# Kernel tuning notes

Measured on AMD Instinct MI355X. Metric: run time of the kernel, lower is better.

Reference implementation:

```python
import jax, jax.numpy as jnp
import numpy as np

NEG_SLOPE = 0.2


def gat_conv(x, edge_index, W, a_src, a_dst, b, heads, ch, concat):
    # PyG GATConv (eval mode, add_self_loops=True).
    # x: [N, Fin]; W: [Fin, heads*ch]; a_src/a_dst: [heads, ch]; b: [heads*ch] or [ch]
    N = x.shape[0]
    loop = jnp.arange(N, dtype=edge_index.dtype)
    src = jnp.concatenate([edge_index[0], loop])
    dst = jnp.concatenate([edge_index[1], loop])
    h = (x @ W).reshape(N, heads, ch)                     # [N,H,C]
    s_src = jnp.sum(h * a_src, axis=-1)                   # [N,H]
    s_dst = jnp.sum(h * a_dst, axis=-1)                   # [N,H]
    e = jax.nn.leaky_relu(s_src[src] + s_dst[dst], NEG_SLOPE)  # [E,H]
    # numerically stable softmax over incoming edges of each dst node
    emax = jax.lax.stop_gradient(jax.ops.segment_max(e, dst, num_segments=N))
    ex = jnp.exp(e - emax[dst])
    denom = jax.ops.segment_sum(ex, dst, num_segments=N) + 1e-16
    alpha = ex / denom[dst]                                # [E,H]
    out = jax.ops.segment_sum(alpha[:, :, None] * h[src], dst, num_segments=N)  # [N,H,C]
    out = out.reshape(N, heads * ch) if concat else out.mean(axis=1)
    return out + b


def setup_inputs() -> dict:
    key = jax.random.key(0)
    N, E, Fin, H, C = 50000, 800000, 64, 8, 16
    D1 = H * C            # 128
    D2 = 3 * D1           # 384
    ks = jax.random.split(key, 40)
    d = {}
    d["X"] = jax.random.normal(ks[0], (N, Fin), dtype=jnp.float32)
    d["A1"] = jax.random.randint(ks[1], (2, E), 0, N, dtype=jnp.int32)
    d["A2"] = jax.random.randint(ks[2], (2, E), 0, N, dtype=jnp.int32)
    d["A3"] = jax.random.randint(ks[3], (2, E), 0, N, dtype=jnp.int32)
    d["edge_feature"] = jax.random.normal(ks[4], (E, 2), dtype=jnp.float32)
    i = 5
    for branch in (1, 2, 3):
        d[f"W{branch}1"] = jax.random.normal(ks[i], (Fin, D1), dtype=jnp.float32) * 0.1; i += 1
        d[f"a_src{branch}1"] = jax.random.normal(ks[i], (H, C), dtype=jnp.float32) * 0.1; i += 1
        d[f"a_dst{branch}1"] = jax.random.normal(ks[i], (H, C), dtype=jnp.float32) * 0.1; i += 1
        d[f"b{branch}1"] = jnp.zeros((D1,), dtype=jnp.float32)
        d[f"W{branch}2"] = jax.random.normal(ks[i], (D2, 1), dtype=jnp.float32) * 0.1; i += 1
        d[f"a_src{branch}2"] = jax.random.normal(ks[i], (1, 1), dtype=jnp.float32) * 0.1; i += 1
        d[f"a_dst{branch}2"] = jax.random.normal(ks[i], (1, 1), dtype=jnp.float32) * 0.1; i += 1
        d[f"b{branch}2"] = jnp.zeros((1,), dtype=jnp.float32)
    d["ln_w"] = jax.random.normal(ks[i], (3, 1), dtype=jnp.float32) * 0.1
    d["ln_b"] = jnp.zeros((1,), dtype=jnp.float32)
    return d


def reference(X, A1, A2, A3, edge_feature,
              W11, a_src11, a_dst11, b11, W12, a_src12, a_dst12, b12,
              W21, a_src21, a_dst21, b21, W22, a_src22, a_dst22, b22,
              W31, a_src31, a_dst31, b31, W32, a_src32, a_dst32, b32,
              ln_w, ln_b):
    H, C = 8, 16
    X1 = jax.nn.relu(gat_conv(X, A1, W11, a_src11, a_dst11, b11, H, C, True))
    X2 = jax.nn.relu(gat_conv(X, A2, W21, a_src21, a_dst21, b21, H, C, True))
    X3 = jax.nn.relu(gat_conv(X, A3, W31, a_src31, a_dst31, b31, H, C, True))
    Xc = jnp.concatenate([X1, X2, X3], axis=1)            # [N, 384]
    Y1 = gat_conv(Xc, A1, W12, a_src12, a_dst12, b12, 1, 1, False)
    Y2 = gat_conv(Xc, A2, W22, a_src22, a_dst22, b22, 1, 1, False)
    Y3 = gat_conv(Xc, A3, W32, a_src32, a_dst32, b32, 1, 1, False)
    Y = jnp.concatenate([Y1, Y2, Y3], axis=1)             # [N, 3]
    return Y @ ln_w + ln_b                                # [N, 1]
```

## Files before the change

### kernel.cpp

```cpp
#include <hip/hip_runtime.h>
#include <cstdint>
#include <cstddef>

#define NEG_SLOPE 0.2f

__device__ __forceinline__ float lrelu(float v) { return v >= 0.f ? v : NEG_SLOPE * v; }

__device__ __forceinline__ unsigned short f2bf(float x) {
    union { float f; uint32_t u; } v; v.f = x;
    uint32_t r = v.u + 0x7FFFu + ((v.u >> 16) & 1u);
    return (unsigned short)(r >> 16);
}
__device__ __forceinline__ float bf2f_lo(uint32_t u) {
    union { uint32_t u; float f; } v; v.u = u << 16;
    return v.f;
}
__device__ __forceinline__ float bf2f_hi(uint32_t u) {
    union { uint32_t u; float f; } v; v.u = u & 0xFFFF0000u;
    return v.f;
}

__device__ __forceinline__ int spreadk(int e) { return (e >> 8) & 7; }

#define L1_NODES 64

__global__ __launch_bounds__(384) void k_lin1_deg(
        const float* __restrict__ X,
        const float* __restrict__ W1, const float* __restrict__ W2,
        const float* __restrict__ W3,
        const float* __restrict__ as1, const float* __restrict__ ad1,
        const float* __restrict__ as2, const float* __restrict__ ad2,
        const float* __restrict__ as3, const float* __restrict__ ad3,
        unsigned short* __restrict__ h_bf,
        float* __restrict__ s_src, float* __restrict__ s_dst,
        const int* __restrict__ A1, const int* __restrict__ A2,
        const int* __restrict__ A3,
        int* __restrict__ deg8, unsigned short* __restrict__ epos,
        int nL1, int nbE, int E, int N) {
    int t = threadIdx.x;
    if (blockIdx.x >= nL1) {
        int b = blockIdx.x - nL1;
        int r = b / nbE;
        int e = (b - r * nbE) * 384 + t;
        if (e < E) {
            const int* A = (r == 0) ? A1 : (r == 1) ? A2 : A3;
            int dst = A[E + e];
            epos[(size_t)r * E + e] =
                (unsigned short)atomicAdd(&deg8[(size_t)((r << 3) + spreadk(e)) * N + dst], 1);
        }
        return;
    }
    __shared__ float Xs[L1_NODES][64];
    int n0 = blockIdx.x * L1_NODES;
    {
        const float4* X4 = reinterpret_cast<const float4*>(X);
        float4* Xs4 = reinterpret_cast<float4*>(&Xs[0][0]);
        for (int i = t; i < L1_NODES * 16; i += 384) {
            int nl = i >> 4;
            float4 xv = make_float4(0.f, 0.f, 0.f, 0.f);
            if (n0 + nl < N) xv = X4[(size_t)(n0 + nl) * 16 + (i & 15)];
            Xs4[i] = xv;
        }
    }
    int r = t >> 7, col = t & 127, head = (t >> 4) & 7, c = t & 15;
    const float* Wp = ((r == 0) ? W1 : (r == 1) ? W2 : W3) + col;
    float Wc[64];
    #pragma unroll
    for (int k = 0; k < 64; ++k) Wc[k] = Wp[(size_t)k * 128];
    float as_v = ((r == 0) ? as1 : (r == 1) ? as2 : as3)[head * 16 + c];
    float ad_v = ((r == 0) ? ad1 : (r == 1) ? ad2 : ad3)[head * 16 + c];
    __syncthreads();
    int nmax = min(L1_NODES, N - n0);
    int rh = (r << 3) + head;
    for (int n = 0; n < nmax; ++n) {
        const float4* xr = reinterpret_cast<const float4*>(&Xs[n][0]);
        float a0 = 0.f, a1 = 0.f, a2 = 0.f, a3 = 0.f;
        #pragma unroll
        for (int k4 = 0; k4 < 16; ++k4) {
            float4 xv = xr[k4];
            a0 = fmaf(xv.x, Wc[k4 * 4 + 0], a0);
            a1 = fmaf(xv.y, Wc[k4 * 4 + 1], a1);
            a2 = fmaf(xv.z, Wc[k4 * 4 + 2], a2);
            a3 = fmaf(xv.w, Wc[k4 * 4 + 3], a3);
        }
        float acc = (a0 + a1) + (a2 + a3);
        h_bf[(size_t)(n0 + n) * 384 + t] = f2bf(acc);
        float ss = acc * as_v, sd = acc * ad_v;
        ss += __shfl_xor(ss, 1); ss += __shfl_xor(ss, 2);
        ss += __shfl_xor(ss, 4); ss += __shfl_xor(ss, 8);
        sd += __shfl_xor(sd, 1); sd += __shfl_xor(sd, 2);
        sd += __shfl_xor(sd, 4); sd += __shfl_xor(sd, 8);
        if (c == 0) {
            s_src[(size_t)(n0 + n) * 24 + rh] = ss;
            s_dst[(size_t)(n0 + n) * 24 + rh] = sd;
        }
    }
}

__global__ void k_scanA2(const int* __restrict__ deg8, int* __restrict__ deg,
                         int* __restrict__ startk, int* __restrict__ start,
                         int* __restrict__ bsum, int total, int N) {
    __shared__ int tmp[256];
    int t = threadIdx.x;
    int base = blockIdx.x * 1024 + t * 4;
    int v[4]; int s = 0;
    #pragma unroll
    for (int m = 0; m < 4; ++m) {
        int g = base + m;
        int sum8 = 0;
        if (g < total) {
            int r = g / N;
            int n = g - r * N;
            #pragma unroll
            for (int k = 0; k < 8; ++k) {
                size_t idx = (size_t)((r << 3) + k) * N + n;
                int dv = deg8[idx];
                startk[idx] = sum8;
                sum8 += dv;
            }
            deg[g] = sum8;
        }
        v[m] = sum8; s += sum8;
    }
    tmp[t] = s; __syncthreads();
    for (int off = 1; off < 256; off <<= 1) {
        int x = (t >= off) ? tmp[t - off] : 0; __syncthreads();
        tmp[t] += x; __syncthreads();
    }
    int run = tmp[t] - s;
    #pragma unroll
    for (int m = 0; m < 4; ++m) {
        if (base + m < total) start[base + m] = run;
        run += v[m];
    }
    if (t == 255) bsum[blockIdx.x] = tmp[255];
}

__global__ void k_scanB(int* __restrict__ bsum, int nb) {
    __shared__ int tmp[256];
    int t = threadIdx.x;
    int v[4]; int s = 0;
    #pragma unroll
    for (int k = 0; k < 4; ++k) { int i = t * 4 + k; v[k] = (i < nb) ? bsum[i] : 0; s += v[k]; }
    tmp[t] = s; __syncthreads();
    for (int off = 1; off < 256; off <<= 1) {
        int x = (t >= off) ? tmp[t - off] : 0; __syncthreads();
        tmp[t] += x; __syncthreads();
    }
    int run = tmp[t] - s;
    #pragma unroll
    for (int k = 0; k < 4; ++k) {
        int i = t * 4 + k;
        if (i < nb) { int vv = v[k]; bsum[i] = run; run += vv; }
    }
}

__global__ void k_scanC2(int* __restrict__ start, const int* __restrict__ bsum,
                         int* __restrict__ startk, float* __restrict__ h2,
                         int total, int N, int E) {
    int g = blockIdx.x * blockDim.x + threadIdx.x;
    if (g >= total) return;
    h2[g] = 0.f;
    int r = g / N;
    int n = g - r * N;
    int base = start[g] + bsum[g >> 10] - r * E;
    start[g] = base;
    #pragma unroll
    for (int k = 0; k < 8; ++k)
        startk[(size_t)((r << 3) + k) * N + n] += base;
}

__global__ void k_scatter2(const int* __restrict__ A1, const int* __restrict__ A2,
                           const int* __restrict__ A3,
                           const int* __restrict__ startk,
                           const unsigned short* __restrict__ epos,
                           unsigned short* __restrict__ csr, int E, int N) {
    int e = blockIdx.x * blockDim.x + threadIdx.x;
    if (e >= E) return;
    int r = blockIdx.y;
    const int* A = (r == 0) ? A1 : (r == 1) ? A2 : A3;
    int src = A[e], dst = A[E + e];
    int pos = startk[(size_t)((r << 3) + spreadk(e)) * N + dst] + epos[(size_t)r * E + e];
    csr[(size_t)r * E + pos] = (unsigned short)src;
}

__global__ __launch_bounds__(64) void k_agg1(
        const unsigned short* __restrict__ h_bf,
        const float* __restrict__ s_src, const float* __restrict__ s_dst,
        const int* __restrict__ deg, const int* __restrict__ start,
        const unsigned short* __restrict__ csr,
        const float* __restrict__ b1, const float* __restrict__ b2,
        const float* __restrict__ b3,
        const float* __restrict__ W12, const float* __restrict__ W22,
        const float* __restrict__ W32,
        float* __restrict__ h2, int E, int N) {
    __shared__ int sidx[64];
    __shared__ float sex[64 * 8];
    int n = blockIdx.x;
    int r = blockIdx.y;
    int j = threadIdx.x;
    int h = j >> 3;
    int rh = r * 8 + h;
    int s0 = start[(size_t)r * N + n];
    int d  = deg[(size_t)r * N + n];
    const uint32_t* hb = reinterpret_cast<const uint32_t*>(h_bf);
    int off = r * 64 + j;
    float sd = s_dst[(size_t)n * 24 + rh];
    float ex0 = __expf(lrelu(s_src[(size_t)n * 24 + rh] + sd));
    float denom = ex0;
    uint32_t hv0 = hb[(size_t)n * 192 + off];
    float accx = ex0 * bf2f_lo(hv0);
    float accy = ex0 * bf2f_hi(hv0);
    int hA = j & 7;
    float sdA = s_dst[(size_t)n * 24 + r * 8 + hA];
    const unsigned short* cs = csr + (size_t)r * E + s0;
    for (int c0 = 0; c0 < d; c0 += 64) {
        int dc = min(64, d - c0);
        if (j < dc) sidx[j] = cs[c0 + j];
        __syncthreads();
        for (int p = j; p < dc * 8; p += 64) {
            int i = p >> 3;
            float ssv = s_src[(size_t)sidx[i] * 24 + r * 8 + hA];
            sex[p] = __expf(lrelu(ssv + sdA));
        }
        __syncthreads();
        for (int i = 0; i < dc; ++i) {
            float ex = sex[i * 8 + h];
            uint32_t hv = hb[(size_t)sidx[i] * 192 + off];
            denom += ex;
            accx = fmaf(ex, bf2f_lo(hv), accx);
            accy = fmaf(ex, bf2f_hi(hv), accy);
        }
        __syncthreads();
    }
    const float* b = (r == 0) ? b1 : (r == 1) ? b2 : b3;
    float inv = 1.0f / (denom + 1e-16f);
    float ox = accx * inv + b[2 * j];
    float oy = accy * inv + b[2 * j + 1];
    ox = (ox > 0.f) ? ox : 0.f;
    oy = (oy > 0.f) ? oy : 0.f;
    int cbase = r * 128 + 2 * j;
    float p0 = ox * W12[cbase] + oy * W12[cbase + 1];
    float p1 = ox * W22[cbase] + oy * W22[cbase + 1];
    float p2 = ox * W32[cbase] + oy * W32[cbase + 1];
    #pragma unroll
    for (int o = 32; o > 0; o >>= 1) {
        p0 += __shfl_xor(p0, o);
        p1 += __shfl_xor(p1, o);
        p2 += __shfl_xor(p2, o);
    }
    if (j == 0) {
        atomicAdd(&h2[(size_t)n * 3 + 0], p0);
        atomicAdd(&h2[(size_t)n * 3 + 1], p1);
        atomicAdd(&h2[(size_t)n * 3 + 2], p2);
    }
}

__global__ __launch_bounds__(384) void k_agg2f(
        const float* __restrict__ h2,
        const int* __restrict__ deg, const int* __restrict__ start,
        const unsigned short* __restrict__ csr,
        const float* __restrict__ as1, const float* __restrict__ ad1,
        const float* __restrict__ as2, const float* __restrict__ ad2,
        const float* __restrict__ as3, const float* __restrict__ ad3,
        const float* __restrict__ b1, const float* __restrict__ b2,
        const float* __restrict__ b3,
        const float* __restrict__ ln_w, const float* __restrict__ ln_b,
        float* __restrict__ out, int E, int N) {
    __shared__ float ys[48];
    int tl = threadIdx.x;
    int pl = tl >> 3;
    int q  = tl & 7;
    int id = blockIdx.x * 48 + pl;
    bool valid = id < 3 * N;
    int n = id / 3;
    int r = id - 3 * n;
    float denom = 0.f, acc = 0.f;
    if (valid) {
        float a_s = ((r == 0) ? as1 : (r == 1) ? as2 : as3)[0];
        float a_d = ((r == 0) ? ad1 : (r == 1) ? ad2 : ad3)[0];
        int s0 = start[(size_t)r * N + n];
        int d  = deg[(size_t)r * N + n];
        float hd = h2[id];
        float sd = a_d * hd;
        const unsigned short* cs = csr + (size_t)r * E + s0;
        for (int i = q; i < d; i += 8) {
            float hs = h2[(size_t)cs[i] * 3 + r];
            float e2 = __expf(lrelu(fmaf(a_s, hs, sd)));
            denom += e2;
            acc = fmaf(e2, hs, acc);
        }
        if (q == 0) {
            float ev = __expf(lrelu(fmaf(a_s, hd, sd)));
            denom += ev;
            acc = fmaf(ev, hd, acc);
        }
    }
    denom += __shfl_xor(denom, 1); denom += __shfl_xor(denom, 2); denom += __shfl_xor(denom, 4);
    acc   += __shfl_xor(acc, 1);   acc   += __shfl_xor(acc, 2);   acc   += __shfl_xor(acc, 4);
    if (valid && q == 0) {
        float b = ((r == 0) ? b1 : (r == 1) ? b2 : b3)[0];
        ys[pl] = (acc / (denom + 1e-16f) + b) * ln_w[r];
    }
    __syncthreads();
    if (valid && q == 0 && r == 0)
        out[n] = ys[pl] + ys[pl + 1] + ys[pl + 2] + ln_b[0];
}

extern "C" void kernel_launch(void* const* d_in, const int* in_sizes, int n_in,
                              void* d_out, int out_size, void* d_ws, size_t ws_size,
                              hipStream_t stream) {
    const float* X  = (const float*)d_in[0];
    const int*   A1 = (const int*)d_in[1];
    const int*   A2 = (const int*)d_in[2];
    const int*   A3 = (const int*)d_in[3];
    const float* W11 = (const float*)d_in[5];
    const float* as11 = (const float*)d_in[6];
    const float* ad11 = (const float*)d_in[7];
    const float* b11 = (const float*)d_in[8];
    const float* W12 = (const float*)d_in[9];
    const float* as12 = (const float*)d_in[10];
    const float* ad12 = (const float*)d_in[11];
    const float* b12 = (const float*)d_in[12];
    const float* W21 = (const float*)d_in[13];
    const float* as21 = (const float*)d_in[14];
    const float* ad21 = (const float*)d_in[15];
    const float* b21 = (const float*)d_in[16];
    const float* W22 = (const float*)d_in[17];
    const float* as22 = (const float*)d_in[18];
    const float* ad22 = (const float*)d_in[19];
    const float* b22 = (const float*)d_in[20];
    const float* W31 = (const float*)d_in[21];
    const float* as31 = (const float*)d_in[22];
    const float* ad31 = (const float*)d_in[23];
    const float* b31 = (const float*)d_in[24];
    const float* W32 = (const float*)d_in[25];
    const float* as32 = (const float*)d_in[26];
    const float* ad32 = (const float*)d_in[27];
    const float* b32 = (const float*)d_in[28];
    const float* ln_w = (const float*)d_in[29];
    const float* ln_b = (const float*)d_in[30];

    const int N = in_sizes[0] / 64;
    const int E = in_sizes[1] / 2;
    const int total = 3 * N;
    const int nbA = (total + 1023) / 1024;
    const int nL1 = (N + L1_NODES - 1) / L1_NODES;
    const int nbE = (E + 383) / 384;

    float* w = (float*)d_ws;
    float* s_src1 = w; w += (size_t)N * 24;
    float* s_dst1 = w; w += (size_t)N * 24;
    float* h2     = w; w += (size_t)N * 3;
    unsigned short* h_bf = (unsigned short*)w; w += (size_t)N * 192;
    int* iw     = (int*)w;
    int* deg    = iw; iw += (size_t)3 * N;
    int* start  = iw; iw += (size_t)3 * N;
    int* bsum   = iw; iw += 1024;
    int* deg8   = iw; iw += (size_t)24 * N;
    int* startk = iw; iw += (size_t)24 * N;
    unsigned short* epos = (unsigned short*)iw;
    unsigned short* csr  = epos + (size_t)3 * E;

    const int BLK = 256;

    hipMemsetAsync(deg8, 0, (size_t)24 * N * sizeof(int), stream);

    k_lin1_deg<<<nL1 + 3 * nbE, 384, 0, stream>>>(
        X, W11, W21, W31, as11, ad11, as21, ad21, as31, ad31,
        h_bf, s_src1, s_dst1,
        A1, A2, A3, deg8, epos, nL1, nbE, E, N);

    k_scanA2<<<nbA, 256, 0, stream>>>(deg8, deg, startk, start, bsum, total, N);
    k_scanB<<<1, 256, 0, stream>>>(bsum, nbA);
    k_scanC2<<<(total + BLK - 1) / BLK, BLK, 0, stream>>>(start, bsum, startk, h2, total, N, E);
    {
        dim3 grid((E + BLK - 1) / BLK, 3);
        k_scatter2<<<grid, BLK, 0, stream>>>(A1, A2, A3, startk, epos, csr, E, N);
    }

    {
        dim3 grid(N, 3);
        k_agg1<<<grid, 64, 0, stream>>>(h_bf, s_src1, s_dst1, deg, start, csr,
                                        b11, b21, b31, W12, W22, W32, h2, E, N);
    }

    {
        int nb = (total + 47) / 48;
        k_agg2f<<<nb, 384, 0, stream>>>(
            h2, deg, start, csr,
            as12, ad12, as22, ad22, as32, ad32,
            b12, b22, b32, ln_w, ln_b, (float*)d_out, E, N);
    }
}
```

Measured before the change: 375.2 us.

## Replace global-atomic CSR build with two-level bucketed counting sort

The CSR construction now uses a two-level counting sort. Edges are first histogrammed per block into buckets of 128 destination nodes using shared-memory atomics, bucket offsets are prefix-summed, and edges are scattered into a packed bucket buffer. A per-bucket kernel then counts and places edges by destination inside each bucket. This replaces the scattered global atomics on the spread degree arrays and the multi-pass scans over 24*N counters. In exchange it adds an intermediate 32-bit edge buffer, more kernel launches, and within-bucket ordering that depends on atomic order.

```diff
diff --git a/kernel.cpp b/kernel.cpp
--- a/kernel.cpp
+++ b/kernel.cpp
@@ -3,6 +3,9 @@
 #include <cstddef>
 
 #define NEG_SLOPE 0.2f
+#define L1_NODES 64
+#define EPT 5
+#define EPB (384 * EPT)
 
 __device__ __forceinline__ float lrelu(float v) { return v >= 0.f ? v : NEG_SLOPE * v; }
 
@@ -20,11 +23,57 @@
     return v.f;
 }
 
-__device__ __forceinline__ int spreadk(int e) { return (e >> 8) & 7; }
-
-#define L1_NODES 64
-
-__global__ __launch_bounds__(384) void k_lin1_deg(
+__global__ __launch_bounds__(384) void k_p1(
+        const int* __restrict__ A1, const int* __restrict__ A2,
+        const int* __restrict__ A3,
+        int* __restrict__ bofs, int nbP, int NB, int E) {
+    __shared__ int hist[512];
+    int t = threadIdx.x, blk = blockIdx.x, r = blockIdx.y;
+    for (int i = t; i < NB; i += 384) hist[i] = 0;
+    __syncthreads();
+    const int* A = (r == 0) ? A1 : (r == 1) ? A2 : A3;
+    int base = blk * EPB;
+    #pragma unroll
+    for (int it = 0; it < EPT; ++it) {
+        int e = base + it * 384 + t;
+        if (e < E) atomicAdd(&hist[A[E + e] >> 7], 1);
+    }
+    __syncthreads();
+    for (int i = t; i < NB; i += 384)
+        bofs[(size_t)(r * nbP + blk) * NB + i] = hist[i];
+}
+
+__global__ __launch_bounds__(512) void k_p2a(
+        int* __restrict__ bofs, int* __restrict__ gbkt, int nbP, int NB) {
+    __shared__ int arr[512];
+    int t = threadIdx.x, b = blockIdx.x, r = blockIdx.y;
+    int v = (t < nbP) ? bofs[(size_t)(r * nbP + t) * NB + b] : 0;
+    arr[t] = v; __syncthreads();
+    for (int off = 1; off < 512; off <<= 1) {
+        int x = (t >= off) ? arr[t - off] : 0; __syncthreads();
+        arr[t] += x; __syncthreads();
+    }
+    if (t < nbP) bofs[(size_t)(r * nbP + t) * NB + b] = arr[t] - v;
+    if (t == 0) gbkt[r * NB + b] = arr[nbP - 1];
+}
+
+__global__ __launch_bounds__(512) void k_p2b(
+        const int* __restrict__ gbkt, int* __restrict__ gstart, int NB) {
+    __shared__ int arr[512];
+    int t = threadIdx.x;
+    for (int r = 0; r < 3; ++r) {
+        int v = (t < NB) ? gbkt[r * NB + t] : 0;
+        arr[t] = v; __syncthreads();
+        for (int off = 1; off < 512; off <<= 1) {
+            int x = (t >= off) ? arr[t - off] : 0; __syncthreads();
+            arr[t] += x; __syncthreads();
+        }
+        if (t < NB) gstart[r * NB + t] = arr[t] - v;
+        __syncthreads();
+    }
+}
+
+__global__ __launch_bounds__(384) void k_p3_lin1(
         const float* __restrict__ X,
         const float* __restrict__ W1, const float* __restrict__ W2,
         const float* __restrict__ W3,
@@ -35,18 +84,31 @@
         float* __restrict__ s_src, float* __restrict__ s_dst,
         const int* __restrict__ A1, const int* __restrict__ A2,
         const int* __restrict__ A3,
-        int* __restrict__ deg8, unsigned short* __restrict__ epos,
-        int nL1, int nbE, int E, int N) {
+        const int* __restrict__ bofs, const int* __restrict__ gstart,
+        uint32_t* __restrict__ ebuf,
+        int nL1, int nbP, int NB, int E, int N) {
     int t = threadIdx.x;
-    if (blockIdx.x >= nL1) {
-        int b = blockIdx.x - nL1;
-        int r = b / nbE;
-        int e = (b - r * nbE) * 384 + t;
-        if (e < E) {
-            const int* A = (r == 0) ? A1 : (r == 1) ? A2 : A3;
-            int dst = A[E + e];
-            epos[(size_t)r * E + e] =
-                (unsigned short)atomicAdd(&deg8[(size_t)((r << 3) + spreadk(e)) * N + dst], 1);
+    if (blockIdx.x >= (unsigned)nL1) {
+        __shared__ int cur[512];
+        int b2 = blockIdx.x - nL1;
+        int r = b2 / nbP, blk = b2 - r * nbP;
+        for (int i = t; i < NB; i += 384) cur[i] = 0;
+        __syncthreads();
+        const int* A = (r == 0) ? A1 : (r == 1) ? A2 : A3;
+        int base = blk * EPB;
+        const int* bo = bofs + (size_t)(r * nbP + blk) * NB;
+        const int* gs = gstart + r * NB;
+        uint32_t* eb = ebuf + (size_t)r * E;
+        #pragma unroll
+        for (int it = 0; it < EPT; ++it) {
+            int e = base + it * 384 + t;
+            if (e < E) {
+                int dst = A[E + e], src = A[e];
+                int b = dst >> 7;
+                int rank = atomicAdd(&cur[b], 1);
+                int pos = gs[b] + bo[b] + rank;
+                eb[pos] = ((uint32_t)src << 7) | (uint32_t)(dst & 127);
+            }
         }
         return;
     }
@@ -97,91 +159,44 @@
     }
 }
 
-__global__ void k_scanA2(const int* __restrict__ deg8, int* __restrict__ deg,
-                         int* __restrict__ startk, int* __restrict__ start,
-                         int* __restrict__ bsum, int total, int N) {
-    __shared__ int tmp[256];
-    int t = threadIdx.x;
-    int base = blockIdx.x * 1024 + t * 4;
-    int v[4]; int s = 0;
+__global__ __launch_bounds__(256) void k_p4(
+        const uint32_t* __restrict__ ebuf,
+        const int* __restrict__ gstart, const int* __restrict__ gbkt,
+        unsigned short* __restrict__ csr,
+        int* __restrict__ deg, int* __restrict__ start,
+        int NB, int E, int N) {
+    __shared__ int dcnt[128], dst_[128], dcur[128], tmp[128];
+    int t = threadIdx.x, b = blockIdx.x, r = blockIdx.y;
+    if (t < 128) { dcnt[t] = 0; dcur[t] = 0; }
+    __syncthreads();
+    int base = gstart[r * NB + b];
+    int m    = gbkt[r * NB + b];
+    const uint32_t* eb = ebuf + (size_t)r * E + base;
+    for (int i = t; i < m; i += 256) atomicAdd(&dcnt[eb[i] & 127], 1);
+    __syncthreads();
+    if (t < 128) tmp[t] = dcnt[t];
+    __syncthreads();
     #pragma unroll
-    for (int m = 0; m < 4; ++m) {
-        int g = base + m;
-        int sum8 = 0;
-        if (g < total) {
-            int r = g / N;
-            int n = g - r * N;
-            #pragma unroll
-            for (int k = 0; k < 8; ++k) {
-                size_t idx = (size_t)((r << 3) + k) * N + n;
-                int dv = deg8[idx];
-                startk[idx] = sum8;
-                sum8 += dv;
-            }
-            deg[g] = sum8;
-        }
-        v[m] = sum8; s += sum8;
-    }
-    tmp[t] = s; __syncthreads();
-    for (int off = 1; off < 256; off <<= 1) {
-        int x = (t >= off) ? tmp[t - off] : 0; __syncthreads();
-        tmp[t] += x; __syncthreads();
-    }
-    int run = tmp[t] - s;
-    #pragma unroll
-    for (int m = 0; m < 4; ++m) {
-        if (base + m < total) start[base + m] = run;
-        run += v[m];
-    }
-    if (t == 255) bsum[blockIdx.x] = tmp[255];
-}
-
-__global__ void k_scanB(int* __restrict__ bsum, int nb) {
-    __shared__ int tmp[256];
-    int t = threadIdx.x;
-    int v[4]; int s = 0;
-    #pragma unroll
-    for (int k = 0; k < 4; ++k) { int i = t * 4 + k; v[k] = (i < nb) ? bsum[i] : 0; s += v[k]; }
-    tmp[t] = s; __syncthreads();
-    for (int off = 1; off < 256; off <<= 1) {
-        int x = (t >= off) ? tmp[t - off] : 0; __syncthreads();
-        tmp[t] += x; __syncthreads();
-    }
-    int run = tmp[t] - s;
-    #pragma unroll
-    for (int k = 0; k < 4; ++k) {
-        int i = t * 4 + k;
-        if (i < nb) { int vv = v[k]; bsum[i] = run; run += vv; }
-    }
-}
-
-__global__ void k_scanC2(int* __restrict__ start, const int* __restrict__ bsum,
-                         int* __restrict__ startk, float* __restrict__ h2,
-                         int total, int N, int E) {
-    int g = blockIdx.x * blockDim.x + threadIdx.x;
-    if (g >= total) return;
-    h2[g] = 0.f;
-    int r = g / N;
-    int n = g - r * N;
-    int base = start[g] + bsum[g >> 10] - r * E;
-    start[g] = base;
-    #pragma unroll
-    for (int k = 0; k < 8; ++k)
-        startk[(size_t)((r << 3) + k) * N + n] += base;
-}
-
-__global__ void k_scatter2(const int* __restrict__ A1, const int* __restrict__ A2,
-                           const int* __restrict__ A3,
-                           const int* __restrict__ startk,
-                           const unsigned short* __restrict__ epos,
-                           unsigned short* __restrict__ csr, int E, int N) {
-    int e = blockIdx.x * blockDim.x + threadIdx.x;
-    if (e >= E) return;
-    int r = blockIdx.y;
-    const int* A = (r == 0) ? A1 : (r == 1) ? A2 : A3;
-    int src = A[e], dst = A[E + e];
-    int pos = startk[(size_t)((r << 3) + spreadk(e)) * N + dst] + epos[(size_t)r * E + e];
-    csr[(size_t)r * E + pos] = (unsigned short)src;
+    for (int off = 1; off < 128; off <<= 1) {
+        int x = (t < 128 && t >= off) ? tmp[t - off] : 0; __syncthreads();
+        if (t < 128) tmp[t] += x; __syncthreads();
+    }
+    if (t < 128) {
+        dst_[t] = tmp[t] - dcnt[t];
+        int node = b * 128 + t;
+        if (node < N) {
+            deg[(size_t)r * N + node]   = dcnt[t];
+            start[(size_t)r * N + node] = base + dst_[t];
+        }
+    }
+    __syncthreads();
+    unsigned short* cs = csr + (size_t)r * E + base;
+    for (int i = t; i < m; i += 256) {
+        uint32_t u = eb[i];
+        int dl = u & 127;
+        int rank = atomicAdd(&dcur[dl], 1);
+        cs[dst_[dl] + rank] = (unsigned short)(u >> 7);
+    }
 }
 
 __global__ __launch_bounds__(64) void k_agg1(
@@ -343,10 +358,9 @@
 
     const int N = in_sizes[0] / 64;
     const int E = in_sizes[1] / 2;
-    const int total = 3 * N;
-    const int nbA = (total + 1023) / 1024;
+    const int NB  = (N + 127) >> 7;
+    const int nbP = (E + EPB - 1) / EPB;
     const int nL1 = (N + L1_NODES - 1) / L1_NODES;
-    const int nbE = (E + 383) / 384;
 
     float* w = (float*)d_ws;
     float* s_src1 = w; w += (size_t)N * 24;
@@ -356,28 +370,22 @@
     int* iw     = (int*)w;
     int* deg    = iw; iw += (size_t)3 * N;
     int* start  = iw; iw += (size_t)3 * N;
-    int* bsum   = iw; iw += 1024;
-    int* deg8   = iw; iw += (size_t)24 * N;
-    int* startk = iw; iw += (size_t)24 * N;
-    unsigned short* epos = (unsigned short*)iw;
-    unsigned short* csr  = epos + (size_t)3 * E;
-
-    const int BLK = 256;
-
-    hipMemsetAsync(deg8, 0, (size_t)24 * N * sizeof(int), stream);
-
-    k_lin1_deg<<<nL1 + 3 * nbE, 384, 0, stream>>>(
+    int* gbkt   = iw; iw += (size_t)3 * NB;
+    int* gstart = iw; iw += (size_t)3 * NB;
+    int* bofs   = iw; iw += (size_t)3 * nbP * NB;
+    uint32_t* ebuf = (uint32_t*)iw; iw += (size_t)3 * E;
+    unsigned short* csr = (unsigned short*)iw;
+
+    hipMemsetAsync(h2, 0, (size_t)3 * N * sizeof(float), stream);
+
+    k_p1<<<dim3(nbP, 3), 384, 0, stream>>>(A1, A2, A3, bofs, nbP, NB, E);
+    k_p2a<<<dim3(NB, 3), 512, 0, stream>>>(bofs, gbkt, nbP, NB);
+    k_p2b<<<1, 512, 0, stream>>>(gbkt, gstart, NB);
+    k_p3_lin1<<<nL1 + 3 * nbP, 384, 0, stream>>>(
         X, W11, W21, W31, as11, ad11, as21, ad21, as31, ad31,
         h_bf, s_src1, s_dst1,
-        A1, A2, A3, deg8, epos, nL1, nbE, E, N);
-
-    k_scanA2<<<nbA, 256, 0, stream>>>(deg8, deg, startk, start, bsum, total, N);
-    k_scanB<<<1, 256, 0, stream>>>(bsum, nbA);
-    k_scanC2<<<(total + BLK - 1) / BLK, BLK, 0, stream>>>(start, bsum, startk, h2, total, N, E);
-    {
-        dim3 grid((E + BLK - 1) / BLK, 3);
-        k_scatter2<<<grid, BLK, 0, stream>>>(A1, A2, A3, startk, epos, csr, E, N);
-    }
+        A1, A2, A3, bofs, gstart, ebuf, nL1, nbP, NB, E, N);
+    k_p4<<<dim3(NB, 3), 256, 0, stream>>>(ebuf, gstart, gbkt, csr, deg, start, NB, E, N);
 
     {
         dim3 grid(N, 3);
@@ -386,7 +394,7 @@
     }
 
     {
-        int nb = (total + 47) / 48;
+        int nb = (3 * N + 47) / 48;
         k_agg2f<<<nb, 384, 0, stream>>>(
             h2, deg, start, csr,
             as12, ad12, as22, ad22, as32, ad32,
```

New measurement: 329.6 us. -12.2%, faster.
